# Performance work log

Hardware: AMD Instinct MI355X
Metric: run time of the kernel (lower is better)

The kernel has to match this reference:

```python
import jax, jax.numpy as jnp
import numpy as np

B, S, D, H = 2, 2048, 1024, 16
DK = D // H
NEG = -1e9


def setup_inputs() -> dict:
    key = jax.random.key(0)
    ks = jax.random.split(key, 12)
    sc = 1.0 / np.sqrt(D)
    inp = {
        "query": jax.random.normal(ks[0], (B, S, D), jnp.float32),
        "key": jax.random.normal(ks[1], (B, S, D), jnp.float32),
        "value": jax.random.normal(ks[2], (B, S, D), jnp.float32),
        "mask": jnp.ones((B, 1, S), jnp.int32),
        "Wq": jax.random.normal(ks[3], (D, D), jnp.float32) * sc,
        "bq": jnp.zeros((D,), jnp.float32),
        "Wk": jax.random.normal(ks[4], (D, D), jnp.float32) * sc,
        "bk": jnp.zeros((D,), jnp.float32),
        "Wv": jax.random.normal(ks[5], (D, D), jnp.float32) * sc,
        "bv": jnp.zeros((D,), jnp.float32),
        "Wo": jax.random.normal(ks[6], (D, D), jnp.float32) * sc,
        "bo": jnp.zeros((D,), jnp.float32),
    }
    return inp


def reference(query, key, value, mask, Wq, bq, Wk, bk, Wv, bv, Wo, bo):
    # projections + split heads: [B,S,D] -> [B,H,S,DK]
    def proj(x, W, b):
        return (x @ W + b).reshape(B, S, H, DK).transpose(0, 2, 1, 3)

    q = proj(query, Wq, bq)
    k = proj(key, Wk, bk)
    v = proj(value, Wv, bv)

    scores = jnp.einsum("bhqd,bhkd->bhqk", q, k) / jnp.sqrt(jnp.float32(DK))
    # mask: [B,1,S] -> unsqueeze head dim -> [B,1,1,S], broadcast over heads & queries
    m = mask[:, None, :, :]  # [B,1,1,S]
    scores = jnp.where(m == 0, NEG, scores)
    p_attn = jax.nn.softmax(scores, axis=-1)  # dropout p=0 (eval)
    x = jnp.einsum("bhqk,bhkd->bhqd", p_attn, v)
    x = x.transpose(0, 2, 1, 3).reshape(B, S, D)
    return x @ Wo + bo
```

## Files before the change

kernel.cpp:

```cpp
#include <hip/hip_runtime.h>
#include <stdint.h>

typedef unsigned short u16;
typedef __bf16 bf16x8 __attribute__((ext_vector_type(8), may_alias));
typedef unsigned short u16x8 __attribute__((ext_vector_type(8), may_alias));
typedef unsigned short u16x4 __attribute__((ext_vector_type(4), may_alias));
typedef float f32x4 __attribute__((ext_vector_type(4)));
typedef float f32x16 __attribute__((ext_vector_type(16)));

__device__ __forceinline__ u16 f2bf(float f) {
    union { float f; uint32_t i; } v; v.f = f;
    return (u16)((v.i + 0x7FFFu + ((v.i >> 16) & 1u)) >> 16);
}

__device__ __forceinline__ float exp2_hw(float x) {
#if __has_builtin(__builtin_amdgcn_exp2f)
    return __builtin_amdgcn_exp2f(x);
#else
    float r; asm("v_exp_f32 %0, %1" : "=v"(r) : "v"(x)); return r;
#endif
}

__device__ __forceinline__ uint32_t cvt_pk_bf16(float a, float b) {
    uint32_t r;
    asm("v_cvt_pk_bf16_f32 %0, %1, %2" : "=v"(r) : "v"(a), "v"(b));
    return r;
}

__device__ __forceinline__ void gld_lds16(const u16* g, u16* l) {
    __builtin_amdgcn_global_load_lds(
        (const __attribute__((address_space(1))) unsigned int*)g,
        (__attribute__((address_space(3))) unsigned int*)l, 16, 0, 0);
}

__global__ __launch_bounds__(256) void cvt_all(
    const float* __restrict__ s0, const float* __restrict__ s1, const float* __restrict__ s2,
    const float* __restrict__ w0, const float* __restrict__ w1,
    const float* __restrict__ w2, const float* __restrict__ w3,
    u16* __restrict__ d0, u16* __restrict__ d1, u16* __restrict__ d2,
    u16* __restrict__ t0, u16* __restrict__ t1,
    u16* __restrict__ t2, u16* __restrict__ t3)
{
    __shared__ float L[64][65];
    const int z = blockIdx.z;
    const int tid = threadIdx.x;
    if (z < 3) {
        const float* s = (z == 0) ? s0 : (z == 1) ? s1 : s2;
        u16*         d = (z == 0) ? d0 : (z == 1) ? d1 : d2;
        const size_t base = ((size_t)blockIdx.x * 256 + tid) * 16;
        #pragma unroll
        for (int p = 0; p < 2; ++p) {
            float4 a = *reinterpret_cast<const float4*>(s + base + p * 8);
            float4 b = *reinterpret_cast<const float4*>(s + base + p * 8 + 4);
            u16x8 o;
            o[0] = f2bf(a.x); o[1] = f2bf(a.y); o[2] = f2bf(a.z); o[3] = f2bf(a.w);
            o[4] = f2bf(b.x); o[5] = f2bf(b.y); o[6] = f2bf(b.z); o[7] = f2bf(b.w);
            *reinterpret_cast<u16x8*>(d + base + p * 8) = o;
        }
    } else {
        if (blockIdx.x >= 256) return;
        const int zi = z - 3;
        const float* w = (zi == 0) ? w0 : (zi == 1) ? w1 : (zi == 2) ? w2 : w3;
        u16*         t = (zi == 0) ? t0 : (zi == 1) ? t1 : (zi == 2) ? t2 : t3;
        const int k0 = (blockIdx.x & 15) * 64, n0 = (blockIdx.x >> 4) * 64;
        const int rr = tid >> 6, cc = tid & 63;
        #pragma unroll
        for (int p = 0; p < 16; ++p)
            L[p * 4 + rr][cc] = w[(size_t)(k0 + p * 4 + rr) * 1024 + n0 + cc];
        __syncthreads();
        #pragma unroll
        for (int p = 0; p < 16; ++p)
            t[(size_t)(n0 + p * 4 + rr) * 1024 + k0 + cc] = f2bf(L[cc][p * 4 + rr]);
    }
}

__global__ __launch_bounds__(256) void gemm_bt(
    const u16* __restrict__ A0, const u16* __restrict__ A1, const u16* __restrict__ A2,
    const u16* __restrict__ B0, const u16* __restrict__ B1, const u16* __restrict__ B2,
    const float* __restrict__ c0, const float* __restrict__ c1, const float* __restrict__ c2,
    void* __restrict__ d0, void* __restrict__ d1, void* __restrict__ d2,
    int mode_override)
{
    __shared__ u16 As[128 * 32];
    __shared__ u16 Bs[128 * 32];

    const int z = blockIdx.z;
    const u16* A = (z == 0) ? A0 : (z == 1) ? A1 : A2;
    const u16* BT = (z == 0) ? B0 : (z == 1) ? B1 : B2;
    const float* bias = (z == 0) ? c0 : (z == 1) ? c1 : c2;
    void* dst = (z == 0) ? d0 : (z == 1) ? d1 : d2;
    const int mode = (mode_override >= 0) ? mode_override : ((z == 2) ? 2 : 0);

    const int tid  = threadIdx.x;
    const int wave = tid >> 6, lane = tid & 63;
    const int quad = lane >> 4, l15 = lane & 15;
    const int row0 = blockIdx.x * 128, col0 = blockIdx.y * 128;
    const int wrow = (wave >> 1) * 64, wcol = (wave & 1) * 64;

    f32x4 acc[4][4] = {};

    for (int k0 = 0; k0 < 1024; k0 += 32) {
        __syncthreads();
        #pragma unroll
        for (int j = 0; j < 2; ++j) {
            const int idx = j * 256 + tid;
            const int r = idx >> 2, kc = (idx & 3) * 8;
            gld_lds16(A  + (size_t)(row0 + r) * 1024 + k0 + kc,
                      &As[(size_t)(j * 256 + wave * 64) * 8]);
            gld_lds16(BT + (size_t)(col0 + r) * 1024 + k0 + kc,
                      &Bs[(size_t)(j * 256 + wave * 64) * 8]);
        }
        __syncthreads();

        bf16x8 a[4], b[4];
        #pragma unroll
        for (int i = 0; i < 4; ++i)
            a[i] = *reinterpret_cast<const bf16x8*>(&As[(wrow + i * 16 + l15) * 32 + quad * 8]);
        #pragma unroll
        for (int j = 0; j < 4; ++j)
            b[j] = *reinterpret_cast<const bf16x8*>(&Bs[(wcol + j * 16 + l15) * 32 + quad * 8]);
        #pragma unroll
        for (int i = 0; i < 4; ++i)
            #pragma unroll
            for (int j = 0; j < 4; ++j)
                acc[i][j] = __builtin_amdgcn_mfma_f32_16x16x32_bf16(a[i], b[j], acc[i][j], 0, 0, 0);
    }

    const float emul = (mode == 0 && z == 0 && mode_override < 0) ? 0.18033688011112042f : 1.0f;

    #pragma unroll
    for (int i = 0; i < 4; ++i) {
        #pragma unroll
        for (int j = 0; j < 4; ++j) {
            const int gc  = col0 + wcol + j * 16 + l15;
            const float bv = bias[gc];
            const int gr0 = row0 + wrow + i * 16 + quad * 4;
            if (mode == 3) {
                float* df = (float*)dst;
                #pragma unroll
                for (int r = 0; r < 4; ++r)
                    df[(size_t)(gr0 + r) * 1024 + gc] = acc[i][j][r] + bv;
            } else if (mode == 2) {
                u16* dp = (u16*)dst;
                const int b = gr0 >> 11, s = gr0 & 2047;
                const int h = gc >> 6,  dk = gc & 63;
                u16x4 pk;
                pk[0] = f2bf(acc[i][j][0] + bv);
                pk[1] = f2bf(acc[i][j][1] + bv);
                pk[2] = f2bf(acc[i][j][2] + bv);
                pk[3] = f2bf(acc[i][j][3] + bv);
                *reinterpret_cast<u16x4*>(dp + ((size_t)((b * 16 + h) * 64 + dk)) * 2048 + s) = pk;
            } else {
                u16* dp = (u16*)dst;
                #pragma unroll
                for (int r = 0; r < 4; ++r) {
                    const int gr = gr0 + r;
                    const int b = gr >> 11, s = gr & 2047;
                    const int h = gc >> 6, dk = gc & 63;
                    dp[((size_t)((b * 16 + h) * 2048 + s)) * 64 + dk] = f2bf((acc[i][j][r] + bv) * emul);
                }
            }
        }
    }
}

__global__ __launch_bounds__(512, 4) void attn_fused(
    const u16* __restrict__ Qb, const u16* __restrict__ Kb,
    const u16* __restrict__ Vt, const int* __restrict__ mask,
    u16* __restrict__ ctx)
{
    __shared__ __align__(16) u16 SMEM[16896];

    const int tid  = threadIdx.x;
    const int w    = tid >> 6;
    const int lane = tid & 63;
    const int l31  = lane & 31;
    const int hi   = lane >> 5;
    const int qw   = w & 3;
    const int kh   = w >> 2;

    const int id = blockIdx.x;
    const int sw = (id & 7) * 64 + (id >> 3);
    const int bh = sw >> 4;
    const int q0 = (sw & 15) * 128;
    const int b  = bh >> 4, h = bh & 15;

    const u16* Qp = Qb + (size_t)bh * 2048 * 64;
    const u16* Kp = Kb + (size_t)bh * 2048 * 64;
    const u16* Vp = Vt + (size_t)bh * 64 * 2048;
    const int* mp = mask + b * 2048;

    bf16x8 qf[4];
    {
        const u16* qrow = Qp + (size_t)(q0 + qw * 32 + l31) * 64 + hi * 8;
        #pragma unroll
        for (int s = 0; s < 4; ++s)
            qf[s] = *reinterpret_cast<const bf16x8*>(qrow + s * 16);
    }

    const int scb = tid & 7, sr = tid >> 3;
    const u16* kg0 = Kp + (size_t)sr * 64 + scb * 8;
    const u16* vg0 = Vp + (size_t)sr * 2048 + scb * 8;
    const int dK = scb * 512 + (sr ^ scb) * 8;

    {
        u16x8 kr = *reinterpret_cast<const u16x8*>(kg0);
        u16x8 vr = *reinterpret_cast<const u16x8*>(vg0);
        *reinterpret_cast<u16x8*>(&SMEM[dK])        = kr;
        *reinterpret_cast<u16x8*>(&SMEM[4096 + dK]) = vr;
    }
    int mreg = mp[lane];
    __syncthreads();

    f32x16 accO0 = {}, accO1 = {};
    float la0 = 0.f, la1 = 0.f, la2 = 0.f, la3 = 0.f;
    const int paddr = (lane ^ 32) << 2;

    int cur = 0;
    for (int t = 0; t < 32; ++t) {
        const int kk = t * 64;
        u16x8 krn, vrn; int mnext = 1;
        if (t < 31) {
            krn = *reinterpret_cast<const u16x8*>(kg0 + (size_t)(kk + 64) * 64);
            vrn = *reinterpret_cast<const u16x8*>(vg0 + (kk + 64));
            mnext = mp[kk + 64 + lane];
        }
        const u16* Kb_ = &SMEM[cur * 8192];
        const u16* Vb_ = &SMEM[cur * 8192 + 4096];

        const bool fullmask = (__ballot(mreg != 0) == ~0ull);

        f32x16 z = {};
        #pragma unroll
        for (int s = 0; s < 4; ++s) {
            const int cb = s * 2 + hi;
            const bf16x8 ak = *reinterpret_cast<const bf16x8*>(
                &Kb_[cb * 512 + (((kh * 32 + l31)) ^ cb) * 8]);
            z = __builtin_amdgcn_mfma_f32_32x32x16_bf16(ak, qf[s], z, 0, 0, 0);
        }
        float p[16];
        #pragma unroll
        for (int r = 0; r < 16; ++r) p[r] = exp2_hw(z[r]);
        if (!fullmask) {
            #pragma unroll
            for (int r = 0; r < 16; ++r) {
                const int kv = kk + kh * 32 + (r & 3) + 8 * (r >> 2) + 4 * hi;
                if (mp[kv] == 0) p[r] = 0.f;
            }
        }
        la0 += p[0] + p[4] + p[8]  + p[12];
        la1 += p[1] + p[5] + p[9]  + p[13];
        la2 += p[2] + p[6] + p[10] + p[14];
        la3 += p[3] + p[7] + p[11] + p[15];

        const uint32_t wd0 = cvt_pk_bf16(p[0],  p[1]);
        const uint32_t wd1 = cvt_pk_bf16(p[2],  p[3]);
        const uint32_t wd2 = cvt_pk_bf16(p[4],  p[5]);
        const uint32_t wd3 = cvt_pk_bf16(p[6],  p[7]);
        const uint32_t wd4 = cvt_pk_bf16(p[8],  p[9]);
        const uint32_t wd5 = cvt_pk_bf16(p[10], p[11]);
        const uint32_t wd6 = cvt_pk_bf16(p[12], p[13]);
        const uint32_t wd7 = cvt_pk_bf16(p[14], p[15]);
        const uint32_t s0 = hi ? wd0 : wd2;
        const uint32_t s1 = hi ? wd1 : wd3;
        const uint32_t s2 = hi ? wd4 : wd6;
        const uint32_t s3 = hi ? wd5 : wd7;
        const uint32_t r0 = (uint32_t)__builtin_amdgcn_ds_bpermute(paddr, (int)s0);
        const uint32_t r1 = (uint32_t)__builtin_amdgcn_ds_bpermute(paddr, (int)s1);
        const uint32_t r2 = (uint32_t)__builtin_amdgcn_ds_bpermute(paddr, (int)s2);
        const uint32_t r3 = (uint32_t)__builtin_amdgcn_ds_bpermute(paddr, (int)s3);
        union { uint32_t u[4]; bf16x8 v; } A0, A1;
        A0.u[0] = hi ? r0  : wd0;
        A0.u[1] = hi ? r1  : wd1;
        A0.u[2] = hi ? wd2 : r0;
        A0.u[3] = hi ? wd3 : r1;
        A1.u[0] = hi ? r2  : wd4;
        A1.u[1] = hi ? r3  : wd5;
        A1.u[2] = hi ? wd6 : r2;
        A1.u[3] = hi ? wd7 : r3;

        const int ck0 = kh * 4 + hi;
        const int ck1 = kh * 4 + 2 + hi;
        const bf16x8 bv00 = *reinterpret_cast<const bf16x8*>(&Vb_[ck0 * 512 + ((     l31) ^ ck0) * 8]);
        const bf16x8 bv01 = *reinterpret_cast<const bf16x8*>(&Vb_[ck1 * 512 + ((     l31) ^ ck1) * 8]);
        const bf16x8 bv10 = *reinterpret_cast<const bf16x8*>(&Vb_[ck0 * 512 + ((32 + l31) ^ ck0) * 8]);
        const bf16x8 bv11 = *reinterpret_cast<const bf16x8*>(&Vb_[ck1 * 512 + ((32 + l31) ^ ck1) * 8]);
        accO0 = __builtin_amdgcn_mfma_f32_32x32x16_bf16(A0.v, bv00, accO0, 0, 0, 0);
        accO0 = __builtin_amdgcn_mfma_f32_32x32x16_bf16(A1.v, bv01, accO0, 0, 0, 0);
        accO1 = __builtin_amdgcn_mfma_f32_32x32x16_bf16(A0.v, bv10, accO1, 0, 0, 0);
        accO1 = __builtin_amdgcn_mfma_f32_32x32x16_bf16(A1.v, bv11, accO1, 0, 0, 0);

        if (t < 31) {
            const int nb = (cur ^ 1) * 8192;
            *reinterpret_cast<u16x8*>(&SMEM[nb + dK])        = krn;
            *reinterpret_cast<u16x8*>(&SMEM[nb + 4096 + dK]) = vrn;
        }
        __syncthreads();
        cur ^= 1;
        mreg = mnext;
    }

    float l_part = (la0 + la1) + (la2 + la3);
    l_part += __shfl_xor(l_part, 32);
    float* F = (float*)SMEM;
    if (kh) {
        #pragma unroll
        for (int r = 0; r < 16; ++r) F[qw * 1024 + r * 64 + lane] = accO0[r];
        #pragma unroll
        for (int r = 0; r < 16; ++r) F[4096 + qw * 1024 + r * 64 + lane] = accO1[r];
        if (lane < 32) F[8192 + qw * 32 + l31] = l_part;
    }
    __syncthreads();
    if (!kh && lane < 32)
        F[8320 + qw * 32 + l31] = 1.0f / (l_part + F[8192 + qw * 32 + l31]);
    __syncthreads();
    if (!kh) {
        #pragma unroll
        for (int r = 0; r < 16; ++r) {
            const int qr = (r & 3) + 8 * (r >> 2) + 4 * hi;
            const float iv = F[8320 + qw * 32 + qr];
            const float o0 = accO0[r] + F[qw * 1024 + r * 64 + lane];
            const float o1 = accO1[r] + F[4096 + qw * 1024 + r * 64 + lane];
            u16* row = ctx + (size_t)(b * 2048 + q0 + qw * 32 + qr) * 1024 + h * 64;
            row[l31]      = f2bf(o0 * iv);
            row[32 + l31] = f2bf(o1 * iv);
        }
    }
}

extern "C" void kernel_launch(void* const* d_in, const int* in_sizes, int n_in,
                              void* d_out, int out_size, void* d_ws, size_t ws_size,
                              hipStream_t stream) {
    const float* query = (const float*)d_in[0];
    const float* key   = (const float*)d_in[1];
    const float* value = (const float*)d_in[2];
    const int*   mask  = (const int*)d_in[3];
    const float* Wq = (const float*)d_in[4];
    const float* bq = (const float*)d_in[5];
    const float* Wk = (const float*)d_in[6];
    const float* bk = (const float*)d_in[7];
    const float* Wv = (const float*)d_in[8];
    const float* bv = (const float*)d_in[9];
    const float* Wo = (const float*)d_in[10];
    const float* bo = (const float*)d_in[11];
    float* out = (float*)d_out;

    u16* ws   = (u16*)d_ws;
    u16* Xq   = ws;
    u16* Xk   = ws + 4194304;
    u16* Xv   = ws + 8388608;
    u16* WqT  = ws + 12582912;
    u16* WkT  = ws + 13631488;
    u16* WvT  = ws + 14680064;
    u16* WoT  = ws + 15728640;
    u16* Qb   = ws + 16777216;
    u16* Kb   = ws + 20971520;
    u16* Vt   = ws + 25165824;
    u16* ctx  = Xq;

    dim3 blk(256);
    cvt_all<<<dim3(1024, 1, 7), blk, 0, stream>>>(query, key, value, Wq, Wk, Wv, Wo,
                                                  Xq, Xk, Xv, WqT, WkT, WvT, WoT);
    gemm_bt<<<dim3(32, 8, 3),  blk, 0, stream>>>(Xq, Xk, Xv, WqT, WkT, WvT,
                                                 bq, bk, bv, Qb, Kb, Vt, -1);
    attn_fused<<<dim3(512), dim3(512), 0, stream>>>(Qb, Kb, Vt, mask, ctx);
    gemm_bt<<<dim3(32, 8, 1),  blk, 0, stream>>>(ctx, ctx, ctx, WoT, WoT, WoT,
                                                 bo, bo, bo, out, out, out, 3);
}
```

Measured before the change: 236.1 us.

## Double-buffer GEMM LDS tiles and XOR-swizzle columns to avoid bank conflicts

The projection GEMM kernel now uses two LDS buffers, prefetching the next K-slice with direct global-to-LDS loads while MFMAs run on the current slice, with one barrier per iteration instead of two. The k-chunk placement within each LDS row is XOR-swizzled by row so the 16-byte fragment reads spread across banks. This doubles LDS use per block, which may reduce occupancy. Correctness depends on the async LDS loads completing before the barrier.

```diff
diff --git a/kernel.cpp b/kernel.cpp
--- a/kernel.cpp
+++ b/kernel.cpp
@@ -81,8 +81,8 @@
     void* __restrict__ d0, void* __restrict__ d1, void* __restrict__ d2,
     int mode_override)
 {
-    __shared__ u16 As[128 * 32];
-    __shared__ u16 Bs[128 * 32];
+    __shared__ u16 As[2 * 4096];
+    __shared__ u16 Bs[2 * 4096];
 
     const int z = blockIdx.z;
     const u16* A = (z == 0) ? A0 : (z == 1) ? A1 : A2;
@@ -97,33 +97,57 @@
     const int row0 = blockIdx.x * 128, col0 = blockIdx.y * 128;
     const int wrow = (wave >> 1) * 64, wcol = (wave & 1) * 64;
 
+    const int sidx0 = tid, sidx1 = 256 + tid;
+    const int sr0 = sidx0 >> 2, sc0 = ((sidx0 & 3) ^ ((sr0 >> 1) & 3)) * 8;
+    const int sr1 = sidx1 >> 2, sc1 = ((sidx1 & 3) ^ ((sr1 >> 1) & 3)) * 8;
+    const size_t aoff0 = (size_t)(row0 + sr0) * 1024 + sc0;
+    const size_t aoff1 = (size_t)(row0 + sr1) * 1024 + sc1;
+    const size_t boff0 = (size_t)(col0 + sr0) * 1024 + sc0;
+    const size_t boff1 = (size_t)(col0 + sr1) * 1024 + sc1;
+    u16* const asl0 = &As[(size_t)(wave * 64) * 8];
+    u16* const asl1 = &As[(size_t)(256 + wave * 64) * 8];
+    u16* const bsl0 = &Bs[(size_t)(wave * 64) * 8];
+    u16* const bsl1 = &Bs[(size_t)(256 + wave * 64) * 8];
+
     f32x4 acc[4][4] = {};
 
+    gld_lds16(A + aoff0, asl0);
+    gld_lds16(BT + boff0, bsl0);
+    gld_lds16(A + aoff1, asl1);
+    gld_lds16(BT + boff1, bsl1);
+    __syncthreads();
+
+    int cur = 0;
     for (int k0 = 0; k0 < 1024; k0 += 32) {
-        __syncthreads();
-        #pragma unroll
-        for (int j = 0; j < 2; ++j) {
-            const int idx = j * 256 + tid;
-            const int r = idx >> 2, kc = (idx & 3) * 8;
-            gld_lds16(A  + (size_t)(row0 + r) * 1024 + k0 + kc,
-                      &As[(size_t)(j * 256 + wave * 64) * 8]);
-            gld_lds16(BT + (size_t)(col0 + r) * 1024 + k0 + kc,
-                      &Bs[(size_t)(j * 256 + wave * 64) * 8]);
-        }
-        __syncthreads();
-
+        if (k0 < 992) {
+            const int nb = (cur ^ 1) * 4096;
+            gld_lds16(A + aoff0 + (k0 + 32), asl0 + nb);
+            gld_lds16(BT + boff0 + (k0 + 32), bsl0 + nb);
+            gld_lds16(A + aoff1 + (k0 + 32), asl1 + nb);
+            gld_lds16(BT + boff1 + (k0 + 32), bsl1 + nb);
+        }
+
+        const u16* Ab = &As[cur * 4096];
+        const u16* Bb = &Bs[cur * 4096];
         bf16x8 a[4], b[4];
         #pragma unroll
-        for (int i = 0; i < 4; ++i)
-            a[i] = *reinterpret_cast<const bf16x8*>(&As[(wrow + i * 16 + l15) * 32 + quad * 8]);
-        #pragma unroll
-        for (int j = 0; j < 4; ++j)
-            b[j] = *reinterpret_cast<const bf16x8*>(&Bs[(wcol + j * 16 + l15) * 32 + quad * 8]);
+        for (int i = 0; i < 4; ++i) {
+            const int ar = wrow + i * 16 + l15;
+            a[i] = *reinterpret_cast<const bf16x8*>(&Ab[ar * 32 + (quad ^ ((ar >> 1) & 3)) * 8]);
+        }
+        #pragma unroll
+        for (int j = 0; j < 4; ++j) {
+            const int br = wcol + j * 16 + l15;
+            b[j] = *reinterpret_cast<const bf16x8*>(&Bb[br * 32 + (quad ^ ((br >> 1) & 3)) * 8]);
+        }
         #pragma unroll
         for (int i = 0; i < 4; ++i)
             #pragma unroll
             for (int j = 0; j < 4; ++j)
                 acc[i][j] = __builtin_amdgcn_mfma_f32_16x16x32_bf16(a[i], b[j], acc[i][j], 0, 0, 0);
+
+        __syncthreads();
+        cur ^= 1;
     }
 
     const float emul = (mode == 0 && z == 0 && mode_override < 0) ? 0.18033688011112042f : 1.0f;
```

Result: faster. 224.8 us (-4.8%).
